# Optimization experiments

Hardware: AMD Instinct MI355X
Metric: run time of the kernel (lower is better)

## Reference

```python
import jax, jax.numpy as jnp
import numpy as np


def _bilinear_sample(tex, grid):
    """grid_sample, bilinear, align_corners=True, padding_mode='zeros'.
    tex: [C, Hin, Win]; grid: [B, Ho, Wo, 2] in [-1, 1] (x=width, y=height).
    Returns [B, C, Ho, Wo].
    """
    C, Hin, Win = tex.shape
    gx, gy = grid[..., 0], grid[..., 1]
    # align_corners=True mapping
    ix = (gx + 1.0) * 0.5 * (Win - 1)
    iy = (gy + 1.0) * 0.5 * (Hin - 1)
    ix0 = jnp.floor(ix)
    iy0 = jnp.floor(iy)
    wx1 = ix - ix0
    wy1 = iy - iy0
    wx0 = 1.0 - wx1
    wy0 = 1.0 - wy1

    def gather(iy_, ix_):
        valid = (ix_ >= 0) & (ix_ <= Win - 1) & (iy_ >= 0) & (iy_ <= Hin - 1)
        ic = jnp.clip(ix_, 0, Win - 1).astype(jnp.int32)
        jc = jnp.clip(iy_, 0, Hin - 1).astype(jnp.int32)
        v = tex[:, jc, ic]  # [C, B, Ho, Wo]
        return v * valid.astype(tex.dtype)[None]

    out = (gather(iy0, ix0) * (wy0 * wx0)[None]
           + gather(iy0, ix0 + 1) * (wy0 * wx1)[None]
           + gather(iy0 + 1, ix0) * (wy1 * wx0)[None]
           + gather(iy0 + 1, ix0 + 1) * (wy1 * wx1)[None])
    return jnp.transpose(out, (1, 0, 2, 3))  # [B, C, Ho, Wo]


def setup_inputs() -> dict:
    key = jax.random.key(0)
    k = jax.random.split(key, 6)
    B, C, W, H = 4, 16, 1024, 1024
    Ho, Wo = 512, 512
    return {
        "x": jax.random.uniform(k[0], (B, Ho, Wo, 2), dtype=jnp.float32),
        "x_msk": jax.random.uniform(k[1], (B, Ho, Wo), dtype=jnp.float32),
        "layer1": jax.random.normal(k[2], (C, W, H), dtype=jnp.float32),
        "layer2": jax.random.normal(k[3], (C, W // 2, H // 2), dtype=jnp.float32),
        "layer3": jax.random.normal(k[4], (C, W // 4, H // 4), dtype=jnp.float32),
        "layer4": jax.random.normal(k[5], (C, W // 8, H // 8), dtype=jnp.float32),
    }


def reference(x, x_msk, layer1, layer2, layer3, layer4):
    grid = x * 2.0 - 1.0
    y = (_bilinear_sample(layer1, grid)
         + _bilinear_sample(layer2, grid)
         + _bilinear_sample(layer3, grid)
         + _bilinear_sample(layer4, grid))
    return y * x_msk[:, None]
```

## Files before the change

kernel.cpp:

```cpp
#include <hip/hip_runtime.h>
#include <hip/hip_fp16.h>

#define CH 16
#define NPIX (4 * 512 * 512)
#define NBINS 4096
#define NBLK_SORT 256
#define PPB (NPIX / NBLK_SORT)
#define SEGS 16

typedef float vfloat4 __attribute__((ext_vector_type(4)));

__global__ __launch_bounds__(256) void interleave_lds2_kernel(
    const float* __restrict__ l1, const float* __restrict__ l2,
    const float* __restrict__ l3, const float* __restrict__ l4,
    __half* __restrict__ w1, __half* __restrict__ w2,
    __half* __restrict__ w3, __half* __restrict__ w4) {
  __shared__ unsigned lds_u[CH][258];
  int b = blockIdx.x;
  const float* src; __half* dst; int HW; size_t tb;
  if (b < 2048)      { src = l1; dst = w1; HW = 1048576; tb = (size_t)b * 512; }
  else if (b < 2560) { src = l2; dst = w2; HW = 262144;  tb = (size_t)(b - 2048) * 512; }
  else if (b < 2688) { src = l3; dst = w3; HW = 65536;   tb = (size_t)(b - 2560) * 512; }
  else               { src = l4; dst = w4; HW = 16384;   tb = (size_t)(b - 2688) * 512; }
  int t = threadIdx.x, lane = t & 63, cg = t >> 6;
#pragma unroll
  for (int j = 0; j < 4; ++j) {
    int c = cg * 4 + j;
    const vfloat4* s4 = (const vfloat4*)(src + (size_t)c * HW + tb);
#pragma unroll
    for (int half_ = 0; half_ < 2; ++half_) {
      vfloat4 v = __builtin_nontemporal_load(&s4[half_ * 64 + lane]);
      unsigned h0 = __half_as_ushort(__float2half(v.x));
      unsigned h1 = __half_as_ushort(__float2half(v.y));
      unsigned h2 = __half_as_ushort(__float2half(v.z));
      unsigned h3 = __half_as_ushort(__float2half(v.w));
      lds_u[c][half_ * 128 + lane * 2 + 0] = h0 | (h1 << 16);
      lds_u[c][half_ * 128 + lane * 2 + 1] = h2 | (h3 << 16);
    }
  }
  __syncthreads();
#pragma unroll
  for (int q = 0; q < 2; ++q) {
    int tt = t + q * 256;
    int idx = tt >> 1, sh = (tt & 1) * 16;
    unsigned o[8];
#pragma unroll
    for (int k = 0; k < 8; ++k) {
      unsigned lo = (lds_u[2 * k + 0][idx] >> sh) & 0xffffu;
      unsigned hi = (lds_u[2 * k + 1][idx] >> sh) & 0xffffu;
      o[k] = lo | (hi << 16);
    }
    uint4* d = (uint4*)(dst + (tb + tt) * CH);
    d[0] = make_uint4(o[0], o[1], o[2], o[3]);
    d[1] = make_uint4(o[4], o[5], o[6], o[7]);
  }
}

__device__ __forceinline__ void sample_layer(const uint4* __restrict__ base,
                                             int W, float u, float v, int h,
                                             float c00, float c01, float c10,
                                             float c11, float acc[8]) {
  float ix = u * (float)(W - 1);
  float iy = v * (float)(W - 1);
  float fx = floorf(ix), fy = floorf(iy);
  float wx1 = ix - fx, wy1 = iy - fy;
  float wx0 = 1.0f - wx1, wy0 = 1.0f - wy1;
  int x0 = min(max((int)fx, 0), W - 1);
  int x1 = min(x0 + 1, W - 1);
  int y0 = min(max((int)fy, 0), W - 1);
  int y1 = min(y0 + 1, W - 1);
  union { uint4 u4; __half2 hh[4]; } a00, a01, a10, a11;
  a00.u4 = base[((size_t)y0 * W + x0) * 2 + h];
  a01.u4 = base[((size_t)y0 * W + x1) * 2 + h];
  a10.u4 = base[((size_t)y1 * W + x0) * 2 + h];
  a11.u4 = base[((size_t)y1 * W + x1) * 2 + h];
  __half2 w00h = __float2half2_rn(wy0 * wx0 * c00);
  __half2 w01h = __float2half2_rn(wy0 * wx1 * c01);
  __half2 w10h = __float2half2_rn(wy1 * wx0 * c10);
  __half2 w11h = __float2half2_rn(wy1 * wx1 * c11);
#pragma unroll
  for (int i = 0; i < 4; ++i) {
    __half2 s = __hmul2(a00.hh[i], w00h);
    s = __hfma2(a01.hh[i], w01h, s);
    s = __hfma2(a10.hh[i], w10h, s);
    s = __hfma2(a11.hh[i], w11h, s);
    float2 f = __half22float2(s);
    acc[2 * i + 0] += f.x;
    acc[2 * i + 1] += f.y;
  }
}

__device__ __forceinline__ void corner_fma(const __half* __restrict__ t,
                                           size_t texel, float w, float acc[CH]) {
  const uint4* q = (const uint4*)(t + texel * CH);
  union { uint4 u; __half2 h[4]; } a, b;
  a.u = q[0];
  b.u = q[1];
#pragma unroll
  for (int i = 0; i < 4; ++i) {
    float2 f = __half22float2(a.h[i]);
    acc[2 * i + 0] = fmaf(f.x, w, acc[2 * i + 0]);
    acc[2 * i + 1] = fmaf(f.y, w, acc[2 * i + 1]);
  }
#pragma unroll
  for (int i = 0; i < 4; ++i) {
    float2 f = __half22float2(b.h[i]);
    acc[8 + 2 * i + 0] = fmaf(f.x, w, acc[8 + 2 * i + 0]);
    acc[8 + 2 * i + 1] = fmaf(f.y, w, acc[8 + 2 * i + 1]);
  }
}

__device__ __forceinline__ void sample_hwc16(const __half* __restrict__ t, int W,
                                             float gx, float gy, float acc[CH]) {
  const float W1 = (float)(W - 1);
  float ix = (gx + 1.0f) * 0.5f * W1;
  float iy = (gy + 1.0f) * 0.5f * W1;
  float ix0f = floorf(ix), iy0f = floorf(iy);
  float wx1 = ix - ix0f, wy1 = iy - iy0f;
  float wx0 = 1.0f - wx1, wy0 = 1.0f - wy1;
  float ix1f = ix0f + 1.0f, iy1f = iy0f + 1.0f;
  float vx0 = (ix0f >= 0.0f && ix0f <= W1) ? 1.0f : 0.0f;
  float vx1 = (ix1f >= 0.0f && ix1f <= W1) ? 1.0f : 0.0f;
  float vy0 = (iy0f >= 0.0f && iy0f <= W1) ? 1.0f : 0.0f;
  float vy1 = (iy1f >= 0.0f && iy1f <= W1) ? 1.0f : 0.0f;
  int x0 = min(max((int)ix0f, 0), W - 1);
  int x1 = min(max((int)ix1f, 0), W - 1);
  int y0 = min(max((int)iy0f, 0), W - 1);
  int y1 = min(max((int)iy1f, 0), W - 1);
  float w00 = wy0 * wx0 * vy0 * vx0;
  float w01 = wy0 * wx1 * vy0 * vx1;
  float w10 = wy1 * wx0 * vy1 * vx0;
  float w11 = wy1 * wx1 * vy1 * vx1;
  corner_fma(t, (size_t)y0 * W + x0, w00, acc);
  corner_fma(t, (size_t)y0 * W + x1, w01, acc);
  corner_fma(t, (size_t)y1 * W + x0, w10, acc);
  corner_fma(t, (size_t)y1 * W + x1, w11, acc);
}

__device__ __forceinline__ int bin_of(float xv, float yv) {
  int bx = min(max((int)(xv * 1023.0f), 0), 1023) >> 4;
  int by = min(max((int)(yv * 1023.0f), 0), 1023) >> 4;
  return (by << 6) + bx;
}

__global__ __launch_bounds__(256) void hist_kernel(
    const float2* __restrict__ x, unsigned* __restrict__ hist) {
  __shared__ unsigned h[NBINS];
  int tid = threadIdx.x, blk = blockIdx.x;
#pragma unroll
  for (int i = 0; i < NBINS / 256; ++i) h[i * 256 + tid] = 0;
  __syncthreads();
  int base = blk * PPB;
#pragma unroll 4
  for (int c = 0; c < PPB / 256; ++c) {
    float2 g = x[base + c * 256 + tid];
    atomicAdd(&h[bin_of(g.x, g.y)], 1u);
  }
  __syncthreads();
#pragma unroll
  for (int i = 0; i < NBINS / 256; ++i)
    hist[(size_t)blk * NBINS + i * 256 + tid] = h[i * 256 + tid];
}

__global__ __launch_bounds__(256) void segsum_kernel(
    const unsigned* __restrict__ hist, unsigned* __restrict__ partial) {
  int gid = blockIdx.x * 256 + threadIdx.x;
  int s = gid >> 12, bin = gid & (NBINS - 1);
  unsigned sum = 0;
#pragma unroll
  for (int k = 0; k < NBLK_SORT / SEGS; ++k)
    sum += hist[(size_t)(s * (NBLK_SORT / SEGS) + k) * NBINS + bin];
  partial[gid] = sum;
}

__global__ __launch_bounds__(256) void segscan_kernel(
    unsigned* __restrict__ partial, unsigned* __restrict__ totals) {
  int bin = blockIdx.x * 256 + threadIdx.x;
  unsigned run = 0;
#pragma unroll
  for (int s = 0; s < SEGS; ++s) {
    unsigned v = partial[s * NBINS + bin];
    partial[s * NBINS + bin] = run;
    run += v;
  }
  totals[bin] = run;
}

__global__ __launch_bounds__(1024) void scan_kernel(
    const unsigned* __restrict__ counts, unsigned* __restrict__ cursor) {
  __shared__ unsigned part[1024];
  int t = threadIdx.x;
  unsigned c0 = counts[4 * t + 0], c1 = counts[4 * t + 1];
  unsigned c2 = counts[4 * t + 2], c3 = counts[4 * t + 3];
  part[t] = c0 + c1 + c2 + c3;
  __syncthreads();
  for (int off = 1; off < 1024; off <<= 1) {
    unsigned v = (t >= off) ? part[t - off] : 0u;
    __syncthreads();
    part[t] += v;
    __syncthreads();
  }
  unsigned base = (t > 0) ? part[t - 1] : 0u;
  cursor[4 * t + 0] = base;
  cursor[4 * t + 1] = base + c0;
  cursor[4 * t + 2] = base + c0 + c1;
  cursor[4 * t + 3] = base + c0 + c1 + c2;
}

__global__ __launch_bounds__(256) void colscan_kernel(
    unsigned* __restrict__ hist, const unsigned* __restrict__ partial,
    const unsigned* __restrict__ binbase) {
  int gid = blockIdx.x * 256 + threadIdx.x;
  int s = gid >> 12, bin = gid & (NBINS - 1);
  unsigned run = partial[s * NBINS + bin] + binbase[bin];
#pragma unroll
  for (int k = 0; k < NBLK_SORT / SEGS; ++k) {
    size_t idx = (size_t)(s * (NBLK_SORT / SEGS) + k) * NBINS + bin;
    unsigned v = hist[idx];
    hist[idx] = run;
    run += v;
  }
}

__global__ __launch_bounds__(256) void scatter2_kernel(
    const float2* __restrict__ x, const float* __restrict__ msk,
    const unsigned* __restrict__ hist, float4* __restrict__ pixrec) {
  __shared__ unsigned cur[NBINS];
  int tid = threadIdx.x, blk = blockIdx.x;
#pragma unroll
  for (int i = 0; i < NBINS / 256; ++i)
    cur[i * 256 + tid] = hist[(size_t)blk * NBINS + i * 256 + tid];
  __syncthreads();
  int base = blk * PPB;
#pragma unroll 4
  for (int c = 0; c < PPB / 256; ++c) {
    int p = base + c * 256 + tid;
    float2 g = x[p];
    float m = msk[p];
    unsigned i = atomicAdd(&cur[bin_of(g.x, g.y)], 1u);
    pixrec[i] = make_float4(g.x, g.y, __uint_as_float((unsigned)p), m);
  }
}

__global__ __launch_bounds__(256) void gather_binned3_kernel(
    const float4* __restrict__ pixrec,
    const __half* __restrict__ t1, const __half* __restrict__ t2,
    const __half* __restrict__ t3, const __half* __restrict__ t4,
    __half* __restrict__ ws2) {
  int bid = blockIdx.x;
  int swz = (bid & 7) * 1024 + (bid >> 3);
  int g = swz * 256 + threadIdx.x;
  int i = g >> 1;
  int h = g & 1;
  float4 r = pixrec[i];
  float u = r.x, v = r.y;
  unsigned p = __float_as_uint(r.z);
  float m = r.w;
  float fx = floorf(u * 1023.0f), fy = floorf(v * 1023.0f);
  float vx0 = (fx >= 0.0f && fx <= 1023.0f) ? 1.0f : 0.0f;
  float vx1 = (fx + 1.0f >= 0.0f && fx + 1.0f <= 1023.0f) ? 1.0f : 0.0f;
  float vy0 = (fy >= 0.0f && fy <= 1023.0f) ? 1.0f : 0.0f;
  float vy1 = (fy + 1.0f >= 0.0f && fy + 1.0f <= 1023.0f) ? 1.0f : 0.0f;
  float c00 = vy0 * vx0, c01 = vy0 * vx1, c10 = vy1 * vx0, c11 = vy1 * vx1;
  float acc[8];
#pragma unroll
  for (int c = 0; c < 8; ++c) acc[c] = 0.0f;
  sample_layer((const uint4*)t1, 1024, u, v, h, c00, c01, c10, c11, acc);
  sample_layer((const uint4*)t2, 512, u, v, h, c00, c01, c10, c11, acc);
  sample_layer((const uint4*)t3, 256, u, v, h, c00, c01, c10, c11, acc);
  sample_layer((const uint4*)t4, 128, u, v, h, c00, c01, c10, c11, acc);
  union { __half2 hh[4]; uint4 u4; } o;
#pragma unroll
  for (int c = 0; c < 4; ++c)
    o.hh[c] = __floats2half2_rn(acc[2 * c] * m, acc[2 * c + 1] * m);
  ((uint4*)(ws2 + (size_t)p * CH))[h] = o.u4;
}

__global__ __launch_bounds__(256) void unscatter16_kernel(
    const __half* __restrict__ ws2, float* __restrict__ out) {
  int t = blockIdx.x * blockDim.x + threadIdx.x;
  int p0 = t * 4;
  int wo = p0 & 511, ho = (p0 >> 9) & 511, b = p0 >> 18;
  const uint4* s = (const uint4*)ws2;
  union { uint4 u[2]; __half2 h[8]; } v[4];
#pragma unroll
  for (int j = 0; j < 4; ++j) {
    v[j].u[0] = s[(size_t)(p0 + j) * 2 + 0];
    v[j].u[1] = s[(size_t)(p0 + j) * 2 + 1];
  }
  size_t obase = (size_t)b * (CH * 262144) + (size_t)ho * 512 + wo;
#pragma unroll
  for (int ch = 0; ch < CH; ++ch) {
    vfloat4 o;
    o.x = __half2float(((ch & 1) ? __high2half(v[0].h[ch >> 1]) : __low2half(v[0].h[ch >> 1])));
    o.y = __half2float(((ch & 1) ? __high2half(v[1].h[ch >> 1]) : __low2half(v[1].h[ch >> 1])));
    o.z = __half2float(((ch & 1) ? __high2half(v[2].h[ch >> 1]) : __low2half(v[2].h[ch >> 1])));
    o.w = __half2float(((ch & 1) ? __high2half(v[3].h[ch >> 1]) : __low2half(v[3].h[ch >> 1])));
    __builtin_nontemporal_store(o, (vfloat4*)(out + obase + (size_t)ch * 262144));
  }
}

__global__ __launch_bounds__(256) void gather_hwc16_kernel(
    const float* __restrict__ x, const float* __restrict__ msk,
    const __half* __restrict__ t1, const __half* __restrict__ t2,
    const __half* __restrict__ t3, const __half* __restrict__ t4,
    float* __restrict__ out) {
  int p = blockIdx.x * blockDim.x + threadIdx.x;
  int wo = p & 511, ho = (p >> 9) & 511, b = p >> 18;
  float2 g = ((const float2*)x)[p];
  float gx = g.x * 2.0f - 1.0f;
  float gy = g.y * 2.0f - 1.0f;
  float m = msk[p];
  float acc[CH];
#pragma unroll
  for (int c = 0; c < CH; ++c) acc[c] = 0.0f;
  sample_hwc16(t1, 1024, gx, gy, acc);
  sample_hwc16(t2, 512, gx, gy, acc);
  sample_hwc16(t3, 256, gx, gy, acc);
  sample_hwc16(t4, 128, gx, gy, acc);
  size_t obase = (size_t)b * (CH * 262144) + (size_t)ho * 512 + wo;
#pragma unroll
  for (int c = 0; c < CH; ++c) out[obase + (size_t)c * 262144] = acc[c] * m;
}

__device__ __forceinline__ void sample_chw(const float* __restrict__ t, int W,
                                           float gx, float gy, float acc[CH]) {
  const float W1 = (float)(W - 1);
  float ix = (gx + 1.0f) * 0.5f * W1;
  float iy = (gy + 1.0f) * 0.5f * W1;
  float ix0f = floorf(ix), iy0f = floorf(iy);
  float wx1 = ix - ix0f, wy1 = iy - iy0f;
  float wx0 = 1.0f - wx1, wy0 = 1.0f - wy1;
  float ix1f = ix0f + 1.0f, iy1f = iy0f + 1.0f;
  float vx0 = (ix0f >= 0.0f && ix0f <= W1) ? 1.0f : 0.0f;
  float vx1 = (ix1f >= 0.0f && ix1f <= W1) ? 1.0f : 0.0f;
  float vy0 = (iy0f >= 0.0f && iy0f <= W1) ? 1.0f : 0.0f;
  float vy1 = (iy1f >= 0.0f && iy1f <= W1) ? 1.0f : 0.0f;
  int x0 = min(max((int)ix0f, 0), W - 1);
  int x1 = min(max((int)ix1f, 0), W - 1);
  int y0 = min(max((int)iy0f, 0), W - 1);
  int y1 = min(max((int)iy1f, 0), W - 1);
  float w00 = wy0 * wx0 * vy0 * vx0;
  float w01 = wy0 * wx1 * vy0 * vx1;
  float w10 = wy1 * wx0 * vy1 * vx0;
  float w11 = wy1 * wx1 * vy1 * vx1;
  size_t HW = (size_t)W * W;
  const float* b00 = t + (size_t)y0 * W + x0;
  const float* b01 = t + (size_t)y0 * W + x1;
  const float* b10 = t + (size_t)y1 * W + x0;
  const float* b11 = t + (size_t)y1 * W + x1;
#pragma unroll
  for (int c = 0; c < CH; ++c) {
    float v00 = b00[c * HW], v01 = b01[c * HW], v10 = b10[c * HW], v11 = b11[c * HW];
    acc[c] = fmaf(v00, w00, fmaf(v01, w01, fmaf(v10, w10, fmaf(v11, w11, acc[c]))));
  }
}

__global__ __launch_bounds__(256) void gather_chw_kernel(
    const float* __restrict__ x, const float* __restrict__ msk,
    const float* __restrict__ l1, const float* __restrict__ l2,
    const float* __restrict__ l3, const float* __restrict__ l4,
    float* __restrict__ out) {
  int p = blockIdx.x * blockDim.x + threadIdx.x;
  int wo = p & 511, ho = (p >> 9) & 511, b = p >> 18;
  float2 g = ((const float2*)x)[p];
  float gx = g.x * 2.0f - 1.0f;
  float gy = g.y * 2.0f - 1.0f;
  float m = msk[p];
  float acc[CH];
#pragma unroll
  for (int c = 0; c < CH; ++c) acc[c] = 0.0f;
  sample_chw(l1, 1024, gx, gy, acc);
  sample_chw(l2, 512, gx, gy, acc);
  sample_chw(l3, 256, gx, gy, acc);
  sample_chw(l4, 128, gx, gy, acc);
  size_t obase = (size_t)b * (CH * 262144) + (size_t)ho * 512 + wo;
#pragma unroll
  for (int c = 0; c < CH; ++c) out[obase + (size_t)c * 262144] = acc[c] * m;
}

extern "C" void kernel_launch(void* const* d_in, const int* in_sizes, int n_in,
                              void* d_out, int out_size, void* d_ws, size_t ws_size,
                              hipStream_t stream) {
  const float* x   = (const float*)d_in[0];
  const float* msk = (const float*)d_in[1];
  const float* l1  = (const float*)d_in[2];
  const float* l2  = (const float*)d_in[3];
  const float* l3  = (const float*)d_in[4];
  const float* l4  = (const float*)d_in[5];
  float* out = (float*)d_out;

  const size_t n_texel = 1048576 + 262144 + 65536 + 16384;
  const size_t tex_bytes = n_texel * CH * sizeof(__half);
  const size_t ws2_bytes = (size_t)NPIX * CH * sizeof(__half);
  const size_t rec_bytes = (size_t)NPIX * sizeof(float4);
  const size_t need_bin  = ws2_bytes + tex_bytes + rec_bytes;
  const size_t need_f16  = tex_bytes;
  const int n_ilv_blocks = (int)(n_texel / 512);

  if (ws_size >= need_bin) {
    char* base = (char*)d_ws;
    __half* ws2    = (__half*)base;
    __half* w1     = (__half*)(base + ws2_bytes);
    __half* w2     = w1 + (size_t)1048576 * CH;
    __half* w3     = w2 + (size_t)262144 * CH;
    __half* w4     = w3 + (size_t)65536 * CH;
    float4* pixrec = (float4*)(base + ws2_bytes + tex_bytes);
    unsigned* hist    = (unsigned*)base;
    unsigned* partial = hist + (size_t)NBLK_SORT * NBINS;
    unsigned* totals  = partial + (size_t)SEGS * NBINS;
    unsigned* binbase = totals + NBINS;

    interleave_lds2_kernel<<<n_ilv_blocks, 256, 0, stream>>>(
        l1, l2, l3, l4, w1, w2, w3, w4);
    hist_kernel<<<NBLK_SORT, 256, 0, stream>>>((const float2*)x, hist);
    segsum_kernel<<<SEGS * NBINS / 256, 256, 0, stream>>>(hist, partial);
    segscan_kernel<<<NBINS / 256, 256, 0, stream>>>(partial, totals);
    scan_kernel<<<1, 1024, 0, stream>>>(totals, binbase);
    colscan_kernel<<<SEGS * NBINS / 256, 256, 0, stream>>>(hist, partial, binbase);
    scatter2_kernel<<<NBLK_SORT, 256, 0, stream>>>((const float2*)x, msk, hist, pixrec);
    gather_binned3_kernel<<<NPIX * 2 / 256, 256, 0, stream>>>(pixrec, w1, w2, w3, w4, ws2);
    unscatter16_kernel<<<NPIX / 4 / 256, 256, 0, stream>>>(ws2, out);
  } else if (ws_size >= need_f16) {
    __half* w1 = (__half*)d_ws;
    __half* w2 = w1 + (size_t)1048576 * CH;
    __half* w3 = w2 + (size_t)262144 * CH;
    __half* w4 = w3 + (size_t)65536 * CH;
    interleave_lds2_kernel<<<n_ilv_blocks, 256, 0, stream>>>(
        l1, l2, l3, l4, w1, w2, w3, w4);
    gather_hwc16_kernel<<<NPIX / 256, 256, 0, stream>>>(x, msk, w1, w2, w3, w4, out);
  } else {
    gather_chw_kernel<<<NPIX / 256, 256, 0, stream>>>(x, msk, l1, l2, l3, l4, out);
  }
}
```

Before: 112.6 us.

## Fuse histogram into interleave kernel, simplify scan, sub-sort pixels within gather blocks

Folds the binning histogram into the texture fp16 interleave launch as extra blocks, so both run in one grid. It replaces the segmented sum/scan/colscan chain with a single column scan over all sort blocks, and adds the bin base inside the scatter kernel. The gather kernel now reorders its 128 pixels by a 4x4 sub-bin key in LDS before sampling, to improve texel locality. The intent is fewer launches and better cache reuse, at the cost of a serial 256-step column scan and extra LDS work and syncs in the gather.

```diff
diff --git a/kernel.cpp b/kernel.cpp
--- a/kernel.cpp
+++ b/kernel.cpp
@@ -6,23 +6,47 @@
 #define NBINS 4096
 #define NBLK_SORT 256
 #define PPB (NPIX / NBLK_SORT)
-#define SEGS 16
+#define NILV 2720
 
 typedef float vfloat4 __attribute__((ext_vector_type(4)));
 
-__global__ __launch_bounds__(256) void interleave_lds2_kernel(
+__device__ __forceinline__ int bin_of(float xv, float yv) {
+  int bx = min(max((int)(xv * 1023.0f), 0), 1023) >> 4;
+  int by = min(max((int)(yv * 1023.0f), 0), 1023) >> 4;
+  return (by << 6) + bx;
+}
+
+__global__ __launch_bounds__(256) void ilv_hist_kernel(
     const float* __restrict__ l1, const float* __restrict__ l2,
     const float* __restrict__ l3, const float* __restrict__ l4,
     __half* __restrict__ w1, __half* __restrict__ w2,
-    __half* __restrict__ w3, __half* __restrict__ w4) {
-  __shared__ unsigned lds_u[CH][258];
-  int b = blockIdx.x;
+    __half* __restrict__ w3, __half* __restrict__ w4,
+    const float2* __restrict__ x, unsigned* __restrict__ hist) {
+  __shared__ unsigned s_lds[CH * 258];
+  int b = blockIdx.x, t = threadIdx.x;
+  if (b >= NILV) {
+    int blk = b - NILV;
+#pragma unroll
+    for (int i = 0; i < NBINS / 256; ++i) s_lds[i * 256 + t] = 0;
+    __syncthreads();
+    int base = blk * PPB;
+#pragma unroll 4
+    for (int c = 0; c < PPB / 256; ++c) {
+      float2 g = x[base + c * 256 + t];
+      atomicAdd(&s_lds[bin_of(g.x, g.y)], 1u);
+    }
+    __syncthreads();
+#pragma unroll
+    for (int i = 0; i < NBINS / 256; ++i)
+      hist[(size_t)blk * NBINS + i * 256 + t] = s_lds[i * 256 + t];
+    return;
+  }
   const float* src; __half* dst; int HW; size_t tb;
   if (b < 2048)      { src = l1; dst = w1; HW = 1048576; tb = (size_t)b * 512; }
   else if (b < 2560) { src = l2; dst = w2; HW = 262144;  tb = (size_t)(b - 2048) * 512; }
   else if (b < 2688) { src = l3; dst = w3; HW = 65536;   tb = (size_t)(b - 2560) * 512; }
   else               { src = l4; dst = w4; HW = 16384;   tb = (size_t)(b - 2688) * 512; }
-  int t = threadIdx.x, lane = t & 63, cg = t >> 6;
+  int lane = t & 63, cg = t >> 6;
 #pragma unroll
   for (int j = 0; j < 4; ++j) {
     int c = cg * 4 + j;
@@ -34,8 +58,8 @@
       unsigned h1 = __half_as_ushort(__float2half(v.y));
       unsigned h2 = __half_as_ushort(__float2half(v.z));
       unsigned h3 = __half_as_ushort(__float2half(v.w));
-      lds_u[c][half_ * 128 + lane * 2 + 0] = h0 | (h1 << 16);
-      lds_u[c][half_ * 128 + lane * 2 + 1] = h2 | (h3 << 16);
+      s_lds[c * 258 + half_ * 128 + lane * 2 + 0] = h0 | (h1 << 16);
+      s_lds[c * 258 + half_ * 128 + lane * 2 + 1] = h2 | (h3 << 16);
     }
   }
   __syncthreads();
@@ -46,13 +70,69 @@
     unsigned o[8];
 #pragma unroll
     for (int k = 0; k < 8; ++k) {
-      unsigned lo = (lds_u[2 * k + 0][idx] >> sh) & 0xffffu;
-      unsigned hi = (lds_u[2 * k + 1][idx] >> sh) & 0xffffu;
+      unsigned lo = (s_lds[(2 * k + 0) * 258 + idx] >> sh) & 0xffffu;
+      unsigned hi = (s_lds[(2 * k + 1) * 258 + idx] >> sh) & 0xffffu;
       o[k] = lo | (hi << 16);
     }
     uint4* d = (uint4*)(dst + (tb + tt) * CH);
     d[0] = make_uint4(o[0], o[1], o[2], o[3]);
     d[1] = make_uint4(o[4], o[5], o[6], o[7]);
+  }
+}
+
+__global__ __launch_bounds__(256) void colscan2_kernel(
+    unsigned* __restrict__ hist, unsigned* __restrict__ totals) {
+  int bin = blockIdx.x * 256 + threadIdx.x;
+  unsigned run = 0;
+  for (int k = 0; k < NBLK_SORT; ++k) {
+    size_t idx = (size_t)k * NBINS + bin;
+    unsigned v = hist[idx];
+    hist[idx] = run;
+    run += v;
+  }
+  totals[bin] = run;
+}
+
+__global__ __launch_bounds__(1024) void scan_kernel(
+    const unsigned* __restrict__ counts, unsigned* __restrict__ cursor) {
+  __shared__ unsigned part[1024];
+  int t = threadIdx.x;
+  unsigned c0 = counts[4 * t + 0], c1 = counts[4 * t + 1];
+  unsigned c2 = counts[4 * t + 2], c3 = counts[4 * t + 3];
+  part[t] = c0 + c1 + c2 + c3;
+  __syncthreads();
+  for (int off = 1; off < 1024; off <<= 1) {
+    unsigned v = (t >= off) ? part[t - off] : 0u;
+    __syncthreads();
+    part[t] += v;
+    __syncthreads();
+  }
+  unsigned base = (t > 0) ? part[t - 1] : 0u;
+  cursor[4 * t + 0] = base;
+  cursor[4 * t + 1] = base + c0;
+  cursor[4 * t + 2] = base + c0 + c1;
+  cursor[4 * t + 3] = base + c0 + c1 + c2;
+}
+
+__global__ __launch_bounds__(256) void scatter2_kernel(
+    const float2* __restrict__ x, const float* __restrict__ msk,
+    const unsigned* __restrict__ hist, const unsigned* __restrict__ binbase,
+    float4* __restrict__ pixrec) {
+  __shared__ unsigned cur[NBINS];
+  int tid = threadIdx.x, blk = blockIdx.x;
+#pragma unroll
+  for (int i = 0; i < NBINS / 256; ++i)
+    cur[i * 256 + tid] = hist[(size_t)blk * NBINS + i * 256 + tid] +
+                         binbase[i * 256 + tid];
+  __syncthreads();
+  int base = blk * PPB;
+#pragma unroll 4
+  for (int c = 0; c < PPB / 256; ++c) {
+    int p = base + c * 256 + tid;
+    float2 g = x[p];
+    float m = msk[p];
+    unsigned i = atomicAdd(&cur[bin_of(g.x, g.y)], 1u);
+    pixrec[i] = make_float4(g.x, g.y, __uint_as_float((unsigned)p), m);
   }
 }
 
@@ -87,6 +167,136 @@
     float2 f = __half22float2(s);
     acc[2 * i + 0] += f.x;
     acc[2 * i + 1] += f.y;
+  }
+}
+
+__global__ __launch_bounds__(256) void gather_binned4_kernel(
+    const float4* __restrict__ pixrec,
+    const __half* __restrict__ t1, const __half* __restrict__ t2,
+    const __half* __restrict__ t3, const __half* __restrict__ t4,
+    __half* __restrict__ ws2) {
+  __shared__ float4 srec[128];
+  __shared__ unsigned qcnt[16];
+  __shared__ unsigned qb[16];
+  __shared__ unsigned char perm[128];
+  int tid = threadIdx.x;
+  int bid = blockIdx.x;
+  int swz = (bid & 7) * 1024 + (bid >> 3);
+  int base = swz * 128;
+  if (tid < 16) qcnt[tid] = 0;
+  __syncthreads();
+  unsigned key = 0, rank = 0;
+  if ((tid & 1) == 0) {
+    int pix = tid >> 1;
+    float4 r = pixrec[base + pix];
+    srec[pix] = r;
+    int tx = min(max((int)(r.x * 1023.0f), 0), 1023);
+    int ty = min(max((int)(r.y * 1023.0f), 0), 1023);
+    key = ((((unsigned)ty >> 2) & 3u) << 2) | (((unsigned)tx >> 2) & 3u);
+    rank = atomicAdd(&qcnt[key], 1u);
+  }
+  __syncthreads();
+  if (tid == 0) {
+    unsigned run = 0;
+#pragma unroll
+    for (int k = 0; k < 16; ++k) { qb[k] = run; run += qcnt[k]; }
+  }
+  __syncthreads();
+  if ((tid & 1) == 0) perm[qb[key] + rank] = (unsigned char)(tid >> 1);
+  __syncthreads();
+  int j = tid >> 1;
+  int h = tid & 1;
+  float4 r = srec[perm[j]];
+  float u = r.x, v = r.y;
+  unsigned p = __float_as_uint(r.z);
+  float m = r.w;
+  float fx = floorf(u * 1023.0f), fy = floorf(v * 1023.0f);
+  float vx0 = (fx >= 0.0f && fx <= 1023.0f) ? 1.0f : 0.0f;
+  float vx1 = (fx + 1.0f >= 0.0f && fx + 1.0f <= 1023.0f) ? 1.0f : 0.0f;
+  float vy0 = (fy >= 0.0f && fy <= 1023.0f) ? 1.0f : 0.0f;
+  float vy1 = (fy + 1.0f >= 0.0f && fy + 1.0f <= 1023.0f) ? 1.0f : 0.0f;
+  float c00 = vy0 * vx0, c01 = vy0 * vx1, c10 = vy1 * vx0, c11 = vy1 * vx1;
+  float acc[8];
+#pragma unroll
+  for (int c = 0; c < 8; ++c) acc[c] = 0.0f;
+  sample_layer((const uint4*)t1, 1024, u, v, h, c00, c01, c10, c11, acc);
+  sample_layer((const uint4*)t2, 512, u, v, h, c00, c01, c10, c11, acc);
+  sample_layer((const uint4*)t3, 256, u, v, h, c00, c01, c10, c11, acc);
+  sample_layer((const uint4*)t4, 128, u, v, h, c00, c01, c10, c11, acc);
+  union { __half2 hh[4]; uint4 u4; } o;
+#pragma unroll
+  for (int c = 0; c < 4; ++c)
+    o.hh[c] = __floats2half2_rn(acc[2 * c] * m, acc[2 * c + 1] * m);
+  ((uint4*)(ws2 + (size_t)p * CH))[h] = o.u4;
+}
+
+__global__ __launch_bounds__(256) void unscatter16_kernel(
+    const __half* __restrict__ ws2, float* __restrict__ out) {
+  int t = blockIdx.x * blockDim.x + threadIdx.x;
+  int p0 = t * 4;
+  int wo = p0 & 511, ho = (p0 >> 9) & 511, b = p0 >> 18;
+  const uint4* s = (const uint4*)ws2;
+  union { uint4 u[2]; __half2 h[8]; } v[4];
+#pragma unroll
+  for (int j = 0; j < 4; ++j) {
+    v[j].u[0] = s[(size_t)(p0 + j) * 2 + 0];
+    v[j].u[1] = s[(size_t)(p0 + j) * 2 + 1];
+  }
+  size_t obase = (size_t)b * (CH * 262144) + (size_t)ho * 512 + wo;
+#pragma unroll
+  for (int ch = 0; ch < CH; ++ch) {
+    vfloat4 o;
+    o.x = __half2float(((ch & 1) ? __high2half(v[0].h[ch >> 1]) : __low2half(v[0].h[ch >> 1])));
+    o.y = __half2float(((ch & 1) ? __high2half(v[1].h[ch >> 1]) : __low2half(v[1].h[ch >> 1])));
+    o.z = __half2float(((ch & 1) ? __high2half(v[2].h[ch >> 1]) : __low2half(v[2].h[ch >> 1])));
+    o.w = __half2float(((ch & 1) ? __high2half(v[3].h[ch >> 1]) : __low2half(v[3].h[ch >> 1])));
+    __builtin_nontemporal_store(o, (vfloat4*)(out + obase + (size_t)ch * 262144));
+  }
+}
+
+__global__ __launch_bounds__(256) void interleave_lds2_kernel(
+    const float* __restrict__ l1, const float* __restrict__ l2,
+    const float* __restrict__ l3, const float* __restrict__ l4,
+    __half* __restrict__ w1, __half* __restrict__ w2,
+    __half* __restrict__ w3, __half* __restrict__ w4) {
+  __shared__ unsigned lds_u[CH][258];
+  int b = blockIdx.x;
+  const float* src; __half* dst; int HW; size_t tb;
+  if (b < 2048)      { src = l1; dst = w1; HW = 1048576; tb = (size_t)b * 512; }
+  else if (b < 2560) { src = l2; dst = w2; HW = 262144;  tb = (size_t)(b - 2048) * 512; }
+  else if (b < 2688) { src = l3; dst = w3; HW = 65536;   tb = (size_t)(b - 2560) * 512; }
+  else               { src = l4; dst = w4; HW = 16384;   tb = (size_t)(b - 2688) * 512; }
+  int t = threadIdx.x, lane = t & 63, cg = t >> 6;
+#pragma unroll
+  for (int j = 0; j < 4; ++j) {
+    int c = cg * 4 + j;
+    const vfloat4* s4 = (const vfloat4*)(src + (size_t)c * HW + tb);
+#pragma unroll
+    for (int half_ = 0; half_ < 2; ++half_) {
+      vfloat4 v = __builtin_nontemporal_load(&s4[half_ * 64 + lane]);
+      unsigned h0 = __half_as_ushort(__float2half(v.x));
+      unsigned h1 = __half_as_ushort(__float2half(v.y));
+      unsigned h2 = __half_as_ushort(__float2half(v.z));
+      unsigned h3 = __half_as_ushort(__float2half(v.w));
+      lds_u[c][half_ * 128 + lane * 2 + 0] = h0 | (h1 << 16);
+      lds_u[c][half_ * 128 + lane * 2 + 1] = h2 | (h3 << 16);
+    }
+  }
+  __syncthreads();
+#pragma unroll
+  for (int q = 0; q < 2; ++q) {
+    int tt = t + q * 256;
+    int idx = tt >> 1, sh = (tt & 1) * 16;
+    unsigned o[8];
+#pragma unroll
+    for (int k = 0; k < 8; ++k) {
+      unsigned lo = (lds_u[2 * k + 0][idx] >> sh) & 0xffffu;
+      unsigned hi = (lds_u[2 * k + 1][idx] >> sh) & 0xffffu;
+      o[k] = lo | (hi << 16);
+    }
+    uint4* d = (uint4*)(dst + (tb + tt) * CH);
+    d[0] = make_uint4(o[0], o[1], o[2], o[3]);
+    d[1] = make_uint4(o[4], o[5], o[6], o[7]);
   }
 }
 
@@ -135,169 +345,6 @@
   corner_fma(t, (size_t)y0 * W + x1, w01, acc);
   corner_fma(t, (size_t)y1 * W + x0, w10, acc);
   corner_fma(t, (size_t)y1 * W + x1, w11, acc);
-}
-
-__device__ __forceinline__ int bin_of(float xv, float yv) {
-  int bx = min(max((int)(xv * 1023.0f), 0), 1023) >> 4;
-  int by = min(max((int)(yv * 1023.0f), 0), 1023) >> 4;
-  return (by << 6) + bx;
-}
-
-__global__ __launch_bounds__(256) void hist_kernel(
-    const float2* __restrict__ x, unsigned* __restrict__ hist) {
-  __shared__ unsigned h[NBINS];
-  int tid = threadIdx.x, blk = blockIdx.x;
-#pragma unroll
-  for (int i = 0; i < NBINS / 256; ++i) h[i * 256 + tid] = 0;
-  __syncthreads();
-  int base = blk * PPB;
-#pragma unroll 4
-  for (int c = 0; c < PPB / 256; ++c) {
-    float2 g = x[base + c * 256 + tid];
-    atomicAdd(&h[bin_of(g.x, g.y)], 1u);
-  }
-  __syncthreads();
-#pragma unroll
-  for (int i = 0; i < NBINS / 256; ++i)
-    hist[(size_t)blk * NBINS + i * 256 + tid] = h[i * 256 + tid];
-}
-
-__global__ __launch_bounds__(256) void segsum_kernel(
-    const unsigned* __restrict__ hist, unsigned* __restrict__ partial) {
-  int gid = blockIdx.x * 256 + threadIdx.x;
-  int s = gid >> 12, bin = gid & (NBINS - 1);
-  unsigned sum = 0;
-#pragma unroll
-  for (int k = 0; k < NBLK_SORT / SEGS; ++k)
-    sum += hist[(size_t)(s * (NBLK_SORT / SEGS) + k) * NBINS + bin];
-  partial[gid] = sum;
-}
-
-__global__ __launch_bounds__(256) void segscan_kernel(
-    unsigned* __restrict__ partial, unsigned* __restrict__ totals) {
-  int bin = blockIdx.x * 256 + threadIdx.x;
-  unsigned run = 0;
-#pragma unroll
-  for (int s = 0; s < SEGS; ++s) {
-    unsigned v = partial[s * NBINS + bin];
-    partial[s * NBINS + bin] = run;
-    run += v;
-  }
-  totals[bin] = run;
-}
-
-__global__ __launch_bounds__(1024) void scan_kernel(
-    const unsigned* __restrict__ counts, unsigned* __restrict__ cursor) {
-  __shared__ unsigned part[1024];
-  int t = threadIdx.x;
-  unsigned c0 = counts[4 * t + 0], c1 = counts[4 * t + 1];
-  unsigned c2 = counts[4 * t + 2], c3 = counts[4 * t + 3];
-  part[t] = c0 + c1 + c2 + c3;
-  __syncthreads();
-  for (int off = 1; off < 1024; off <<= 1) {
-    unsigned v = (t >= off) ? part[t - off] : 0u;
-    __syncthreads();
-    part[t] += v;
-    __syncthreads();
-  }
-  unsigned base = (t > 0) ? part[t - 1] : 0u;
-  cursor[4 * t + 0] = base;
-  cursor[4 * t + 1] = base + c0;
-  cursor[4 * t + 2] = base + c0 + c1;
-  cursor[4 * t + 3] = base + c0 + c1 + c2;
-}
-
-__global__ __launch_bounds__(256) void colscan_kernel(
-    unsigned* __restrict__ hist, const unsigned* __restrict__ partial,
-    const unsigned* __restrict__ binbase) {
-  int gid = blockIdx.x * 256 + threadIdx.x;
-  int s = gid >> 12, bin = gid & (NBINS - 1);
-  unsigned run = partial[s * NBINS + bin] + binbase[bin];
-#pragma unroll
-  for (int k = 0; k < NBLK_SORT / SEGS; ++k) {
-    size_t idx = (size_t)(s * (NBLK_SORT / SEGS) + k) * NBINS + bin;
-    unsigned v = hist[idx];
-    hist[idx] = run;
-    run += v;
-  }
-}
-
-__global__ __launch_bounds__(256) void scatter2_kernel(
-    const float2* __restrict__ x, const float* __restrict__ msk,
-    const unsigned* __restrict__ hist, float4* __restrict__ pixrec) {
-  __shared__ unsigned cur[NBINS];
-  int tid = threadIdx.x, blk = blockIdx.x;
-#pragma unroll
-  for (int i = 0; i < NBINS / 256; ++i)
-    cur[i * 256 + tid] = hist[(size_t)blk * NBINS + i * 256 + tid];
-  __syncthreads();
-  int base = blk * PPB;
-#pragma unroll 4
-  for (int c = 0; c < PPB / 256; ++c) {
-    int p = base + c * 256 + tid;
-    float2 g = x[p];
-    float m = msk[p];
-    unsigned i = atomicAdd(&cur[bin_of(g.x, g.y)], 1u);
-    pixrec[i] = make_float4(g.x, g.y, __uint_as_float((unsigned)p), m);
-  }
-}
-
-__global__ __launch_bounds__(256) void gather_binned3_kernel(
-    const float4* __restrict__ pixrec,
-    const __half* __restrict__ t1, const __half* __restrict__ t2,
-    const __half* __restrict__ t3, const __half* __restrict__ t4,
-    __half* __restrict__ ws2) {
-  int bid = blockIdx.x;
-  int swz = (bid & 7) * 1024 + (bid >> 3);
-  int g = swz * 256 + threadIdx.x;
-  int i = g >> 1;
-  int h = g & 1;
-  float4 r = pixrec[i];
-  float u = r.x, v = r.y;
-  unsigned p = __float_as_uint(r.z);
-  float m = r.w;
-  float fx = floorf(u * 1023.0f), fy = floorf(v * 1023.0f);
-  float vx0 = (fx >= 0.0f && fx <= 1023.0f) ? 1.0f : 0.0f;
-  float vx1 = (fx + 1.0f >= 0.0f && fx + 1.0f <= 1023.0f) ? 1.0f : 0.0f;
-  float vy0 = (fy >= 0.0f && fy <= 1023.0f) ? 1.0f : 0.0f;
-  float vy1 = (fy + 1.0f >= 0.0f && fy + 1.0f <= 1023.0f) ? 1.0f : 0.0f;
-  float c00 = vy0 * vx0, c01 = vy0 * vx1, c10 = vy1 * vx0, c11 = vy1 * vx1;
-  float acc[8];
-#pragma unroll
-  for (int c = 0; c < 8; ++c) acc[c] = 0.0f;
-  sample_layer((const uint4*)t1, 1024, u, v, h, c00, c01, c10, c11, acc);
-  sample_layer((const uint4*)t2, 512, u, v, h, c00, c01, c10, c11, acc);
-  sample_layer((const uint4*)t3, 256, u, v, h, c00, c01, c10, c11, acc);
-  sample_layer((const uint4*)t4, 128, u, v, h, c00, c01, c10, c11, acc);
-  union { __half2 hh[4]; uint4 u4; } o;
-#pragma unroll
-  for (int c = 0; c < 4; ++c)
-    o.hh[c] = __floats2half2_rn(acc[2 * c] * m, acc[2 * c + 1] * m);
-  ((uint4*)(ws2 + (size_t)p * CH))[h] = o.u4;
-}
-
-__global__ __launch_bounds__(256) void unscatter16_kernel(
-    const __half* __restrict__ ws2, float* __restrict__ out) {
-  int t = blockIdx.x * blockDim.x + threadIdx.x;
-  int p0 = t * 4;
-  int wo = p0 & 511, ho = (p0 >> 9) & 511, b = p0 >> 18;
-  const uint4* s = (const uint4*)ws2;
-  union { uint4 u[2]; __half2 h[8]; } v[4];
-#pragma unroll
-  for (int j = 0; j < 4; ++j) {
-    v[j].u[0] = s[(size_t)(p0 + j) * 2 + 0];
-    v[j].u[1] = s[(size_t)(p0 + j) * 2 + 1];
-  }
-  size_t obase = (size_t)b * (CH * 262144) + (size_t)ho * 512 + wo;
-#pragma unroll
-  for (int ch = 0; ch < CH; ++ch) {
-    vfloat4 o;
-    o.x = __half2float(((ch & 1) ? __high2half(v[0].h[ch >> 1]) : __low2half(v[0].h[ch >> 1])));
-    o.y = __half2float(((ch & 1) ? __high2half(v[1].h[ch >> 1]) : __low2half(v[1].h[ch >> 1])));
-    o.z = __half2float(((ch & 1) ? __high2half(v[2].h[ch >> 1]) : __low2half(v[2].h[ch >> 1])));
-    o.w = __half2float(((ch & 1) ? __high2half(v[3].h[ch >> 1]) : __low2half(v[3].h[ch >> 1])));
-    __builtin_nontemporal_store(o, (vfloat4*)(out + obase + (size_t)ch * 262144));
-  }
 }
 
 __global__ __launch_bounds__(256) void gather_hwc16_kernel(
@@ -396,7 +443,6 @@
   const size_t rec_bytes = (size_t)NPIX * sizeof(float4);
   const size_t need_bin  = ws2_bytes + tex_bytes + rec_bytes;
   const size_t need_f16  = tex_bytes;
-  const int n_ilv_blocks = (int)(n_texel / 512);
 
   if (ws_size >= need_bin) {
     char* base = (char*)d_ws;
@@ -407,26 +453,24 @@
     __half* w4     = w3 + (size_t)65536 * CH;
     float4* pixrec = (float4*)(base + ws2_bytes + tex_bytes);
     unsigned* hist    = (unsigned*)base;
-    unsigned* partial = hist + (size_t)NBLK_SORT * NBINS;
-    unsigned* totals  = partial + (size_t)SEGS * NBINS;
+    unsigned* totals  = hist + (size_t)NBLK_SORT * NBINS;
     unsigned* binbase = totals + NBINS;
 
-    interleave_lds2_kernel<<<n_ilv_blocks, 256, 0, stream>>>(
-        l1, l2, l3, l4, w1, w2, w3, w4);
-    hist_kernel<<<NBLK_SORT, 256, 0, stream>>>((const float2*)x, hist);
-    segsum_kernel<<<SEGS * NBINS / 256, 256, 0, stream>>>(hist, partial);
-    segscan_kernel<<<NBINS / 256, 256, 0, stream>>>(partial, totals);
+    ilv_hist_kernel<<<NILV + NBLK_SORT, 256, 0, stream>>>(
+        l1, l2, l3, l4, w1, w2, w3, w4, (const float2*)x, hist);
+    colscan2_kernel<<<NBINS / 256, 256, 0, stream>>>(hist, totals);
     scan_kernel<<<1, 1024, 0, stream>>>(totals, binbase);
-    colscan_kernel<<<SEGS * NBINS / 256, 256, 0, stream>>>(hist, partial, binbase);
-    scatter2_kernel<<<NBLK_SORT, 256, 0, stream>>>((const float2*)x, msk, hist, pixrec);
-    gather_binned3_kernel<<<NPIX * 2 / 256, 256, 0, stream>>>(pixrec, w1, w2, w3, w4, ws2);
+    scatter2_kernel<<<NBLK_SORT, 256, 0, stream>>>(
+        (const float2*)x, msk, hist, binbase, pixrec);
+    gather_binned4_kernel<<<NPIX / 128, 256, 0, stream>>>(
+        pixrec, w1, w2, w3, w4, ws2);
     unscatter16_kernel<<<NPIX / 4 / 256, 256, 0, stream>>>(ws2, out);
   } else if (ws_size >= need_f16) {
     __half* w1 = (__half*)d_ws;
     __half* w2 = w1 + (size_t)1048576 * CH;
     __half* w3 = w2 + (size_t)262144 * CH;
     __half* w4 = w3 + (size_t)65536 * CH;
-    interleave_lds2_kernel<<<n_ilv_blocks, 256, 0, stream>>>(
+    interleave_lds2_kernel<<<(int)(n_texel / 512), 256, 0, stream>>>(
         l1, l2, l3, l4, w1, w2, w3, w4);
     gather_hwc16_kernel<<<NPIX / 256, 256, 0, stream>>>(x, msk, w1, w2, w3, w4, out);
   } else {
```

After: 108.0 us. -4.0%, faster.
